# Kernel tuning notes

Hardware: AMD Instinct MI355X
Metric: run time of the kernel (lower is better)

The kernel has to match this reference:

```python
import jax, jax.numpy as jnp
import numpy as np

B, C, T, HEADS = 4, 1024, 1024, 16


def setup_inputs() -> dict:
    key = jax.random.key(0)
    k0, k1, k2, k3 = jax.random.split(key, 4)
    x = jax.random.normal(k0, (B, C, T), dtype=jnp.float32)
    mask = jax.random.randint(k1, (B, T), 0, 2).astype(bool)  # True = masked position
    scale = 1.0 / np.sqrt(C).astype(np.float32)
    w_kvq = jax.random.normal(k2, (3 * C, C), dtype=jnp.float32) * scale  # Conv1d k=1, no bias
    w_out = jax.random.normal(k3, (C, C), dtype=jnp.float32) * scale
    return {"x": x, "mask": mask, "w_kvq": w_kvq, "w_out": w_out}


def reference(x, mask, w_kvq, w_out):
    b, c, t = x.shape
    h = HEADS
    d = c // h  # head dim; torch scales by sqrt(k.size(1)) = sqrt(d)
    # Conv1d with kernel 1 == per-timestep matmul over channels
    kvq = jnp.einsum('oc,bct->bot', w_kvq, x)  # [B, 3C, T]
    k, v, q = jnp.split(kvq, 3, axis=1)        # each [B, C, T]
    k = k.reshape(b, h, d, t)
    v = v.reshape(b, h, d, t)
    q = q.reshape(b, h, d, t)
    # att[b,h,i,j] = <k_i, q_j> / sqrt(d); i = key pos, j = query pos
    att = jnp.einsum('bhdi,bhdj->bhij', k, q) / jnp.sqrt(jnp.asarray(d, x.dtype))
    # pre-softmax: mask key positions (dim i) with -inf
    att = jnp.where(mask[:, None, :, None], -jnp.inf, att)
    att = jax.nn.softmax(att, axis=2)  # softmax over keys (torch dim=1 of [Bh,Tk,Tq])
    # post-softmax: zero out masked query positions (dim j)
    att = jnp.where(mask[:, None, None, :], jnp.asarray(0.0, x.dtype), att)
    o = jnp.einsum('bhdi,bhij->bhdj', v, att)  # [B, h, d, T]
    o = o.reshape(b, c, t)
    out = x + jnp.einsum('oc,bct->bot', w_out, o)
    # match torch layout: cat over heads along batch dim -> [h*B, T, T]
    att_flat = jnp.transpose(att, (1, 0, 2, 3)).reshape(h * b, t, t)
    return out, att_flat
```

## Files before the change

kernel.cpp:

```cpp
#include <hip/hip_runtime.h>

#define BB 4
#define CC 1024
#define TT 1024
#define HH 16
#define DD 64

typedef __bf16 v8bf __attribute__((ext_vector_type(8)));
typedef __bf16 v4bf __attribute__((ext_vector_type(4)));
typedef float  v4f  __attribute__((ext_vector_type(4)));

__device__ __forceinline__ void async16(const __bf16* g, __bf16* l) {
  __builtin_amdgcn_global_load_lds(
      (const __attribute__((address_space(1))) void*)g,
      (__attribute__((address_space(3))) void*)l, 16, 0, 0);
}

__global__ __launch_bounds__(256) void expand_mask_kernel(const void* mraw, float* maskf) {
  __shared__ int flagA, flagB;
  if (threadIdx.x == 0) { flagA = 0; flagB = 0; }
  __syncthreads();
  const unsigned char* mb = (const unsigned char*)mraw;
  const int n = BB * TT;
  int a = 0, bfl = 0;
  for (int i = threadIdx.x; i < n; i += 256) {
    if (mb[i]) { if ((i & 3) == 0) a = 1; else bfl = 1; }
  }
  if (a)   atomicOr(&flagA, 1);
  if (bfl) atomicOr(&flagB, 1);
  __syncthreads();
  int layout;
  if (flagA && !flagB)      layout = 0;
  else if (!flagA && flagB) layout = 1;
  else                      layout = 2;
  for (int i = threadIdx.x; i < n; i += 256) {
    float m;
    if (layout == 0)      m = (((const int*)mraw)[i]   != 0)   ? 1.f : 0.f;
    else if (layout == 1) m = (((const float*)mraw)[i] != 0.f) ? 1.f : 0.f;
    else                  m = (mb[i] != 0)                     ? 1.f : 0.f;
    maskf[i] = m;
  }
}

__global__ __launch_bounds__(256) void cast_f32_bf16(const float* __restrict__ src,
                                                     __bf16* __restrict__ dst, int n) {
  int i = (blockIdx.x * 256 + threadIdx.x) * 8;
  if (i >= n) return;
  float4 f0 = *(const float4*)(src + i);
  float4 f1 = *(const float4*)(src + i + 4);
  v8bf o;
  o[0] = (__bf16)f0.x; o[1] = (__bf16)f0.y; o[2] = (__bf16)f0.z; o[3] = (__bf16)f0.w;
  o[4] = (__bf16)f1.x; o[5] = (__bf16)f1.y; o[6] = (__bf16)f1.z; o[7] = (__bf16)f1.w;
  *(v8bf*)(dst + i) = o;
}

__global__ __launch_bounds__(256) void transpose_x(const float* __restrict__ x,
                                                   __bf16* __restrict__ xT) {
  const int b = blockIdx.z;
  const int t0 = blockIdx.x * 64, c0 = blockIdx.y * 64;
  __shared__ __bf16 T[64][72];
  const int tid = threadIdx.x;
  {
    int row = tid >> 2, coff = (tid & 3) * 16;
    const float* src = x + ((long)b * CC + c0 + row) * TT + t0 + coff;
#pragma unroll
    for (int s = 0; s < 4; s++) {
      float4 f = *(const float4*)(src + s * 4);
      T[row][coff + s * 4 + 0] = (__bf16)f.x;
      T[row][coff + s * 4 + 1] = (__bf16)f.y;
      T[row][coff + s * 4 + 2] = (__bf16)f.z;
      T[row][coff + s * 4 + 3] = (__bf16)f.w;
    }
  }
  __syncthreads();
  {
    int trow = tid >> 2, ccoff = (tid & 3) * 16;
    __bf16 vals[16];
#pragma unroll
    for (int i = 0; i < 16; i++) vals[i] = T[ccoff + i][trow];
    __bf16* dst = xT + ((long)b * TT + t0 + trow) * CC + c0 + ccoff;
    *(v8bf*)dst       = *(v8bf*)&vals[0];
    *(v8bf*)(dst + 8) = *(v8bf*)&vals[8];
  }
}

__global__ __launch_bounds__(256) void transpose_kq(const __bf16* __restrict__ kvqb,
                                                    __bf16* __restrict__ kqT) {
  const int zz = blockIdx.z;
  const int b = zz >> 1, part = zz & 1;
  const int srcbase = part == 0 ? 0 : 2 * CC;
  const int dstbase = part * CC;
  const int t0 = blockIdx.x * 64, c0 = blockIdx.y * 64;
  __shared__ __bf16 T[64][72];
  const int tid = threadIdx.x;
  {
    int row = tid >> 2, coff = (tid & 3) * 16;
    const __bf16* src = kvqb + ((long)b * 3 * CC + srcbase + c0 + row) * TT + t0 + coff;
    *(v8bf*)&T[row][coff]     = *(const v8bf*)src;
    *(v8bf*)&T[row][coff + 8] = *(const v8bf*)(src + 8);
  }
  __syncthreads();
  {
    int trow = tid >> 2, ccoff = (tid & 3) * 16;
    __bf16 vals[16];
#pragma unroll
    for (int i = 0; i < 16; i++) vals[i] = T[ccoff + i][trow];
    __bf16* dst = kqT + ((long)b * TT + t0 + trow) * (2 * CC) + dstbase + c0 + ccoff;
    *(v8bf*)dst       = *(v8bf*)&vals[0];
    *(v8bf*)(dst + 8) = *(v8bf*)&vals[8];
  }
}

template <int MODE>
__global__ __launch_bounds__(256) void gemm_bt(
    const __bf16* __restrict__ A, const __bf16* __restrict__ BTfull,
    const float* __restrict__ Sfull, void* __restrict__ Ofull,
    long strideBT, long strideOS)
{
  const __bf16* BT = BTfull + (long)blockIdx.z * strideBT;
  const int m0 = blockIdx.y * 128, n0 = blockIdx.x * 128;
  __shared__ __align__(16) __bf16 As[128 * 32];
  __shared__ __align__(16) __bf16 Bs[128 * 32];
  const int tid = threadIdx.x;
  const int lane = tid & 63, wave = tid >> 6;
  const int wm = wave >> 1, wn = wave & 1;
  const int ln = lane & 15, q = lane >> 4;

  v4f acc[4][4];
#pragma unroll
  for (int i = 0; i < 4; i++)
#pragma unroll
    for (int j = 0; j < 4; j++) acc[i][j] = (v4f)(0.f);

  const int e0 = tid * 8;
  const int r0 = e0 >> 5, c0 = e0 & 31;
  const int e1 = (256 + tid) * 8;
  const int r1 = e1 >> 5, c1 = e1 & 31;
  const __bf16* ga0 = A  + (long)(m0 + r0) * CC + c0;
  const __bf16* ga1 = A  + (long)(m0 + r1) * CC + c1;
  const __bf16* gb0 = BT + (long)(n0 + r0) * CC + c0;
  const __bf16* gb1 = BT + (long)(n0 + r1) * CC + c1;
  __bf16* lA0 = &As[wave * 512];
  __bf16* lA1 = &As[2048 + wave * 512];
  __bf16* lB0 = &Bs[wave * 512];
  __bf16* lB1 = &Bs[2048 + wave * 512];

  for (int k0 = 0; k0 < CC; k0 += 32) {
    async16(ga0 + k0, lA0);
    async16(ga1 + k0, lA1);
    async16(gb0 + k0, lB0);
    async16(gb1 + k0, lB1);
    __syncthreads();
    v8bf af[4], bfr[4];
#pragma unroll
    for (int mi = 0; mi < 4; mi++)
      af[mi] = *(v8bf*)&As[(wm * 64 + mi * 16 + ln) * 32 + q * 8];
#pragma unroll
    for (int ni = 0; ni < 4; ni++)
      bfr[ni] = *(v8bf*)&Bs[(wn * 64 + ni * 16 + ln) * 32 + q * 8];
#pragma unroll
    for (int mi = 0; mi < 4; mi++)
#pragma unroll
      for (int ni = 0; ni < 4; ni++)
        acc[mi][ni] = __builtin_amdgcn_mfma_f32_16x16x32_bf16(af[mi], bfr[ni], acc[mi][ni], 0, 0, 0);
    __syncthreads();
  }
#pragma unroll
  for (int mi = 0; mi < 4; mi++)
#pragma unroll
    for (int ni = 0; ni < 4; ni++)
#pragma unroll
      for (int r = 0; r < 4; r++) {
        int row = m0 + wm * 64 + mi * 16 + q * 4 + r;
        int col = n0 + wn * 64 + ni * 16 + ln;
        if (MODE == 0) {
          ((__bf16*)Ofull)[(long)blockIdx.z * strideOS + (long)row * TT + col] = (__bf16)acc[mi][ni][r];
        } else {
          long off = (long)blockIdx.z * strideOS + (long)row * TT + col;
          ((float*)Ofull)[off] = acc[mi][ni][r] + Sfull[off];
        }
      }
}

__global__ __launch_bounds__(256) void attn_stats(
    const __bf16* __restrict__ kqT, const float* __restrict__ maskf,
    float* __restrict__ psum)
{
  const int z = blockIdx.z, h = z >> 2, b = z & 3;
  const int i0 = blockIdx.y * 128, j0 = blockIdx.x * 128;
  __shared__ __bf16 Ks[128][72];
  __shared__ __bf16 Qs[128][72];
  const __bf16* kbase = kqT + (long)b * TT * (2 * CC);
  const int tid = threadIdx.x;
#pragma unroll
  for (int s = 0; s < 4; s++) {
    int c = tid + s * 256;
    int row = c >> 3, off = (c & 7) * 8;
    *(v8bf*)&Ks[row][off] = *(const v8bf*)(kbase + (long)(i0 + row) * (2 * CC) + h * DD + off);
    *(v8bf*)&Qs[row][off] = *(const v8bf*)(kbase + (long)(j0 + row) * (2 * CC) + CC + h * DD + off);
  }
  __syncthreads();
  const int lane = tid & 63, wave = tid >> 6;
  const int wi = wave >> 1, wj = wave & 1;
  const int ln = lane & 15, q = lane >> 4;

  v8bf ak[4][2], bq[4][2];
#pragma unroll
  for (int mi = 0; mi < 4; mi++)
#pragma unroll
    for (int kd = 0; kd < 2; kd++)
      ak[mi][kd] = *(v8bf*)&Ks[wi * 64 + mi * 16 + ln][kd * 32 + q * 8];
#pragma unroll
  for (int ni = 0; ni < 4; ni++)
#pragma unroll
    for (int kd = 0; kd < 2; kd++)
      bq[ni][kd] = *(v8bf*)&Qs[wj * 64 + ni * 16 + ln][kd * 32 + q * 8];

  v4f acc[4][4];
#pragma unroll
  for (int mi = 0; mi < 4; mi++)
#pragma unroll
    for (int ni = 0; ni < 4; ni++) {
      v4f a = (v4f)(0.f);
      a = __builtin_amdgcn_mfma_f32_16x16x32_bf16(ak[mi][0], bq[ni][0], a, 0, 0, 0);
      a = __builtin_amdgcn_mfma_f32_16x16x32_bf16(ak[mi][1], bq[ni][1], a, 0, 0, 0);
      acc[mi][ni] = a;
    }

  float kmv[4][4];
#pragma unroll
  for (int mi = 0; mi < 4; mi++)
#pragma unroll
    for (int r = 0; r < 4; r++)
      kmv[mi][r] = maskf[b * TT + i0 + wi * 64 + mi * 16 + q * 4 + r];

#pragma unroll
  for (int ni = 0; ni < 4; ni++) {
    float s = 0.f;
#pragma unroll
    for (int mi = 0; mi < 4; mi++)
#pragma unroll
      for (int r = 0; r < 4; r++) {
        float e = __expf(acc[mi][ni][r] * 0.125f);
        s += (kmv[mi][r] != 0.f) ? 0.f : e;
      }
    s += __shfl_xor(s, 16, 64);
    s += __shfl_xor(s, 32, 64);
    if (q == 0) {
      long so = ((long)z * 16 + (i0 >> 6) + wi) * TT + j0 + wj * 64 + ni * 16 + ln;
      psum[so] = s;
    }
  }
}

__global__ __launch_bounds__(256) void gemm_pv(
    const __bf16* __restrict__ kqT, const __bf16* __restrict__ kvqb,
    const float* __restrict__ psum, const float* __restrict__ maskf,
    float* __restrict__ att, __bf16* __restrict__ oT)
{
  const int z = blockIdx.y, h = z >> 2, b = z & 3;
  const int j0 = blockIdx.x * 64;
  __shared__ __align__(16) char smem[40960];
  float* km = (float*)smem;
  const int tid = threadIdx.x;
  const int lane = tid & 63, wave = tid >> 6;
  const int ln = lane & 15, q = lane >> 4;
  __bf16 (*Pt)[72] = (__bf16(*)[72])(smem + 4096 + wave * 9216);

  const __bf16* kbase = kqT + (long)b * TT * (2 * CC);
  const __bf16* vbase = kvqb + (long)(b * 3 * CC + CC + h * DD) * TT;

  {
    float4 f = *(const float4*)(maskf + b * TT + tid * 4);
    *(float4*)&km[tid * 4] = f;
  }
  __syncthreads();

  v8bf bq[4][2];
#pragma unroll
  for (int ni = 0; ni < 4; ni++) {
    const __bf16* qr = kbase + (long)(j0 + ni * 16 + ln) * (2 * CC) + CC + h * DD;
    bq[ni][0] = *(const v8bf*)(qr + q * 8);
    bq[ni][1] = *(const v8bf*)(qr + 32 + q * 8);
  }
  float st[4];
#pragma unroll
  for (int ni = 0; ni < 4; ni++) {
    int j = j0 + ni * 16 + ln;
    float S = 0.f;
#pragma unroll
    for (int t = 0; t < 16; t++) S += psum[((long)z * 16 + t) * TT + j];
    st[ni] = (km[j] != 0.f) ? 0.f : 1.f / S;
  }

  v4f acc[4][4];
#pragma unroll
  for (int i = 0; i < 4; i++)
#pragma unroll
    for (int j = 0; j < 4; j++) acc[i][j] = (v4f)(0.f);

  for (int it = 0; it < 4; it++) {
    const int ibase = wave * 256 + it * 64;
#pragma unroll
    for (int mi = 0; mi < 4; mi++) {
      const __bf16* arow = kbase + (long)(ibase + mi * 16 + ln) * (2 * CC) + h * DD;
      v8bf ak0 = *(const v8bf*)(arow + q * 8);
      v8bf ak1 = *(const v8bf*)(arow + 32 + q * 8);
#pragma unroll
      for (int ni = 0; ni < 4; ni++) {
        v4f l4 = (v4f)(0.f);
        l4 = __builtin_amdgcn_mfma_f32_16x16x32_bf16(ak0, bq[ni][0], l4, 0, 0, 0);
        l4 = __builtin_amdgcn_mfma_f32_16x16x32_bf16(ak1, bq[ni][1], l4, 0, 0, 0);
        v4bf pb;
#pragma unroll
        for (int r = 0; r < 4; r++) {
          int i_loc = mi * 16 + q * 4 + r;
          int i_glob = ibase + i_loc;
          float p = (km[i_glob] != 0.f) ? 0.f : __expf(l4[r] * 0.125f) * st[ni];
          att[((long)z << 20) + (long)i_glob * TT + j0 + ni * 16 + ln] = p;
          pb[r] = (__bf16)p;
        }
        *(v4bf*)&Pt[ni * 16 + ln][mi * 16 + q * 4] = pb;
      }
    }
    v8bf ap[4][2], bv[4][2];
#pragma unroll
    for (int ji = 0; ji < 4; ji++)
#pragma unroll
      for (int ki = 0; ki < 2; ki++)
        ap[ji][ki] = *(v8bf*)&Pt[ji * 16 + ln][ki * 32 + q * 8];
#pragma unroll
    for (int di = 0; di < 4; di++)
#pragma unroll
      for (int ki = 0; ki < 2; ki++)
        bv[di][ki] = *(const v8bf*)(vbase + (long)(di * 16 + ln) * TT + ibase + ki * 32 + q * 8);
#pragma unroll
    for (int ji = 0; ji < 4; ji++)
#pragma unroll
      for (int di = 0; di < 4; di++) {
        acc[ji][di] = __builtin_amdgcn_mfma_f32_16x16x32_bf16(ap[ji][0], bv[di][0], acc[ji][di], 0, 0, 0);
        acc[ji][di] = __builtin_amdgcn_mfma_f32_16x16x32_bf16(ap[ji][1], bv[di][1], acc[ji][di], 0, 0, 0);
      }
  }

  float (*red0)[68] = (float(*)[68])(smem + 4096);
  float (*red1)[68] = (float(*)[68])(smem + 21504);
  __syncthreads();
  if ((wave & 1) == 0) {
    float (*red)[68] = (wave == 0) ? red0 : red1;
#pragma unroll
    for (int ji = 0; ji < 4; ji++)
#pragma unroll
      for (int di = 0; di < 4; di++)
#pragma unroll
        for (int r = 0; r < 4; r++)
          red[ji * 16 + q * 4 + r][di * 16 + ln] = acc[ji][di][r];
  }
  __syncthreads();
  if ((wave & 1) == 1) {
    float (*red)[68] = (wave == 1) ? red0 : red1;
#pragma unroll
    for (int ji = 0; ji < 4; ji++)
#pragma unroll
      for (int di = 0; di < 4; di++)
#pragma unroll
        for (int r = 0; r < 4; r++)
          red[ji * 16 + q * 4 + r][di * 16 + ln] += acc[ji][di][r];
  }
  __syncthreads();
  {
    int row = tid >> 2, c0 = (tid & 3) * 16;
    __bf16 ob[16];
#pragma unroll
    for (int i = 0; i < 16; i++) ob[i] = (__bf16)(red0[row][c0 + i] + red1[row][c0 + i]);
    __bf16* dst = oT + ((long)b * TT + j0 + row) * CC + h * DD + c0;
    *(v8bf*)dst       = *(v8bf*)&ob[0];
    *(v8bf*)(dst + 8) = *(v8bf*)&ob[8];
  }
}

extern "C" void kernel_launch(void* const* d_in, const int* in_sizes, int n_in,
                              void* d_out, int out_size, void* d_ws, size_t ws_size,
                              hipStream_t stream) {
  const float* x     = (const float*)d_in[0];
  const void*  mask  = d_in[1];
  const float* w_kvq = (const float*)d_in[2];
  const float* w_out = (const float*)d_in[3];

  float* out = (float*)d_out;
  float* att = out + (long)BB * CC * TT;

  char* wsb = (char*)d_ws;
  float*   maskf = (float*)(wsb + 0);
  __bf16*  wkb   = (__bf16*)(wsb + 16384);
  __bf16*  wob   = (__bf16*)(wsb + 6307840);
  __bf16*  xT    = (__bf16*)(wsb + 8404992);
  __bf16*  kqT   = (__bf16*)(wsb + 8404992);
  __bf16*  kvqb  = (__bf16*)(wsb + 25182208);
  __bf16*  oT    = (__bf16*)(wsb + 50348032);
  float*   psum  = (float*)(wsb + 58736640);

  expand_mask_kernel<<<1, 256, 0, stream>>>(mask, maskf);
  cast_f32_bf16<<<(3 * CC * CC) / 2048, 256, 0, stream>>>(w_kvq, wkb, 3 * CC * CC);
  cast_f32_bf16<<<(CC * CC) / 2048, 256, 0, stream>>>(w_out, wob, CC * CC);
  transpose_x<<<dim3(16, 16, BB), 256, 0, stream>>>(x, xT);
  gemm_bt<0><<<dim3(8, 24, BB), 256, 0, stream>>>(
      wkb, xT, nullptr, kvqb, (long)CC * TT, (long)3 * CC * TT);
  transpose_kq<<<dim3(16, 16, 2 * BB), 256, 0, stream>>>(kvqb, kqT);
  attn_stats<<<dim3(8, 8, HH * BB), 256, 0, stream>>>(kqT, maskf, psum);
  gemm_pv<<<dim3(16, HH * BB), 256, 0, stream>>>(kqT, kvqb, psum, maskf, att, oT);
  gemm_bt<1><<<dim3(8, 8, BB), 256, 0, stream>>>(
      wob, oT, x, out, (long)CC * TT, (long)CC * TT);
}
```

Before: 458.8 us.

## Fuse prep kernels, remap block order for XCDs, bitpack key mask, add setprio

Merges the mask expansion, the two weight casts and the x transpose into one prep launch, which also builds a bit-packed key mask. The GEMM, stats and PV kernels remap their flat block index so that neighbouring tiles land on the same XCD, which should improve L2 reuse. attn_stats now loads K and Q fragments straight from global memory instead of staging them in LDS. gemm_pv computes the per-query normaliser once per block in shared memory, reads mask bits instead of floats, and raises wave priority around the MFMA sections. Together these cut launch count and some memory traffic, at the cost of more complex indexing and uncoalesced direct loads in attn_stats.

```diff
diff --git a/kernel.cpp b/kernel.cpp
--- a/kernel.cpp
+++ b/kernel.cpp
@@ -16,71 +16,85 @@
       (__attribute__((address_space(3))) void*)l, 16, 0, 0);
 }
 
-__global__ __launch_bounds__(256) void expand_mask_kernel(const void* mraw, float* maskf) {
+__global__ __launch_bounds__(256) void prep(
+    const void* mraw, float* __restrict__ maskf, unsigned int* __restrict__ kmb,
+    const float* __restrict__ w_kvq, const float* __restrict__ w_out,
+    __bf16* __restrict__ wkb, __bf16* __restrict__ wob,
+    const float* __restrict__ x, __bf16* __restrict__ xT)
+{
+  const int blk = blockIdx.x;
+  const int tid = threadIdx.x;
   __shared__ int flagA, flagB;
-  if (threadIdx.x == 0) { flagA = 0; flagB = 0; }
-  __syncthreads();
-  const unsigned char* mb = (const unsigned char*)mraw;
-  const int n = BB * TT;
-  int a = 0, bfl = 0;
-  for (int i = threadIdx.x; i < n; i += 256) {
-    if (mb[i]) { if ((i & 3) == 0) a = 1; else bfl = 1; }
-  }
-  if (a)   atomicOr(&flagA, 1);
-  if (bfl) atomicOr(&flagB, 1);
-  __syncthreads();
-  int layout;
-  if (flagA && !flagB)      layout = 0;
-  else if (!flagA && flagB) layout = 1;
-  else                      layout = 2;
-  for (int i = threadIdx.x; i < n; i += 256) {
-    float m;
-    if (layout == 0)      m = (((const int*)mraw)[i]   != 0)   ? 1.f : 0.f;
-    else if (layout == 1) m = (((const float*)mraw)[i] != 0.f) ? 1.f : 0.f;
-    else                  m = (mb[i] != 0)                     ? 1.f : 0.f;
-    maskf[i] = m;
-  }
-}
-
-__global__ __launch_bounds__(256) void cast_f32_bf16(const float* __restrict__ src,
-                                                     __bf16* __restrict__ dst, int n) {
-  int i = (blockIdx.x * 256 + threadIdx.x) * 8;
-  if (i >= n) return;
-  float4 f0 = *(const float4*)(src + i);
-  float4 f1 = *(const float4*)(src + i + 4);
-  v8bf o;
-  o[0] = (__bf16)f0.x; o[1] = (__bf16)f0.y; o[2] = (__bf16)f0.z; o[3] = (__bf16)f0.w;
-  o[4] = (__bf16)f1.x; o[5] = (__bf16)f1.y; o[6] = (__bf16)f1.z; o[7] = (__bf16)f1.w;
-  *(v8bf*)(dst + i) = o;
-}
-
-__global__ __launch_bounds__(256) void transpose_x(const float* __restrict__ x,
-                                                   __bf16* __restrict__ xT) {
-  const int b = blockIdx.z;
-  const int t0 = blockIdx.x * 64, c0 = blockIdx.y * 64;
   __shared__ __bf16 T[64][72];
-  const int tid = threadIdx.x;
-  {
-    int row = tid >> 2, coff = (tid & 3) * 16;
-    const float* src = x + ((long)b * CC + c0 + row) * TT + t0 + coff;
-#pragma unroll
-    for (int s = 0; s < 4; s++) {
-      float4 f = *(const float4*)(src + s * 4);
-      T[row][coff + s * 4 + 0] = (__bf16)f.x;
-      T[row][coff + s * 4 + 1] = (__bf16)f.y;
-      T[row][coff + s * 4 + 2] = (__bf16)f.z;
-      T[row][coff + s * 4 + 3] = (__bf16)f.w;
-    }
-  }
-  __syncthreads();
-  {
-    int trow = tid >> 2, ccoff = (tid & 3) * 16;
-    __bf16 vals[16];
-#pragma unroll
-    for (int i = 0; i < 16; i++) vals[i] = T[ccoff + i][trow];
-    __bf16* dst = xT + ((long)b * TT + t0 + trow) * CC + c0 + ccoff;
-    *(v8bf*)dst       = *(v8bf*)&vals[0];
-    *(v8bf*)(dst + 8) = *(v8bf*)&vals[8];
+
+  if (blk == 0) {
+    if (tid == 0) { flagA = 0; flagB = 0; }
+    __syncthreads();
+    const unsigned char* mb = (const unsigned char*)mraw;
+    const int n = BB * TT;
+    int a = 0, bfl = 0;
+    for (int i = tid; i < n; i += 256) {
+      if (mb[i]) { if ((i & 3) == 0) a = 1; else bfl = 1; }
+    }
+    if (a)   atomicOr(&flagA, 1);
+    if (bfl) atomicOr(&flagB, 1);
+    __syncthreads();
+    int layout;
+    if (flagA && !flagB)      layout = 0;
+    else if (!flagA && flagB) layout = 1;
+    else                      layout = 2;
+    const int lane = tid & 63, wave = tid >> 6;
+    for (int it = 0; it < 16; it++) {
+      int i = it * 256 + tid;
+      float m;
+      if (layout == 0)      m = (((const int*)mraw)[i]   != 0)   ? 1.f : 0.f;
+      else if (layout == 1) m = (((const float*)mraw)[i] != 0.f) ? 1.f : 0.f;
+      else                  m = (mb[i] != 0)                     ? 1.f : 0.f;
+      maskf[i] = m;
+      unsigned long long bal = __ballot(m != 0.f);
+      if (lane == 0) {
+        int base = (it * 256 + wave * 64) >> 5;
+        kmb[base]     = (unsigned int)bal;
+        kmb[base + 1] = (unsigned int)(bal >> 32);
+      }
+    }
+  } else if (blk <= 2048) {
+    const int cb = blk - 1;
+    const float* src; __bf16* dst; int base;
+    if (cb < 1536) { src = w_kvq; dst = wkb; base = cb * 2048; }
+    else           { src = w_out; dst = wob; base = (cb - 1536) * 2048; }
+    int i = base + tid * 8;
+    float4 f0 = *(const float4*)(src + i);
+    float4 f1 = *(const float4*)(src + i + 4);
+    v8bf o;
+    o[0] = (__bf16)f0.x; o[1] = (__bf16)f0.y; o[2] = (__bf16)f0.z; o[3] = (__bf16)f0.w;
+    o[4] = (__bf16)f1.x; o[5] = (__bf16)f1.y; o[6] = (__bf16)f1.z; o[7] = (__bf16)f1.w;
+    *(v8bf*)(dst + i) = o;
+  } else {
+    const int idx = blk - 2049;
+    const int t0 = (idx & 15) * 64, c0 = ((idx >> 4) & 15) * 64, b = idx >> 8;
+    {
+      int row = tid >> 2, coff = (tid & 3) * 16;
+      const float* src = x + ((long)b * CC + c0 + row) * TT + t0 + coff;
+#pragma unroll
+      for (int s = 0; s < 4; s++) {
+        float4 f = *(const float4*)(src + s * 4);
+        T[row][coff + s * 4 + 0] = (__bf16)f.x;
+        T[row][coff + s * 4 + 1] = (__bf16)f.y;
+        T[row][coff + s * 4 + 2] = (__bf16)f.z;
+        T[row][coff + s * 4 + 3] = (__bf16)f.w;
+      }
+    }
+    __syncthreads();
+    {
+      int trow = tid >> 2, ccoff = (tid & 3) * 16;
+      __bf16 vals[16];
+#pragma unroll
+      for (int i = 0; i < 16; i++) vals[i] = T[ccoff + i][trow];
+      __bf16* dst = xT + ((long)b * TT + t0 + trow) * CC + c0 + ccoff;
+      *(v8bf*)dst       = *(v8bf*)&vals[0];
+      *(v8bf*)(dst + 8) = *(v8bf*)&vals[8];
+    }
   }
 }
 
@@ -111,14 +125,19 @@
   }
 }
 
-template <int MODE>
+template <int MODE, int NB, int MB>
 __global__ __launch_bounds__(256) void gemm_bt(
     const __bf16* __restrict__ A, const __bf16* __restrict__ BTfull,
     const float* __restrict__ Sfull, void* __restrict__ Ofull,
     long strideBT, long strideOS)
 {
-  const __bf16* BT = BTfull + (long)blockIdx.z * strideBT;
-  const int m0 = blockIdx.y * 128, n0 = blockIdx.x * 128;
+  constexpr int TOT = NB * MB * BB;
+  int flat = blockIdx.x + NB * (blockIdx.y + MB * blockIdx.z);
+  int L = (flat & 7) * (TOT / 8) + (flat >> 3);
+  const int n0 = (L % NB) * 128;
+  const int m0 = ((L / NB) % MB) * 128;
+  const int zb = L / (NB * MB);
+  const __bf16* BT = BTfull + (long)zb * strideBT;
   __shared__ __align__(16) __bf16 As[128 * 32];
   __shared__ __align__(16) __bf16 Bs[128 * 32];
   const int tid = threadIdx.x;
@@ -174,9 +193,9 @@
         int row = m0 + wm * 64 + mi * 16 + q * 4 + r;
         int col = n0 + wn * 64 + ni * 16 + ln;
         if (MODE == 0) {
-          ((__bf16*)Ofull)[(long)blockIdx.z * strideOS + (long)row * TT + col] = (__bf16)acc[mi][ni][r];
+          ((__bf16*)Ofull)[(long)zb * strideOS + (long)row * TT + col] = (__bf16)acc[mi][ni][r];
         } else {
-          long off = (long)blockIdx.z * strideOS + (long)row * TT + col;
+          long off = (long)zb * strideOS + (long)row * TT + col;
           ((float*)Ofull)[off] = acc[mi][ni][r] + Sfull[off];
         }
       }
@@ -186,37 +205,33 @@
     const __bf16* __restrict__ kqT, const float* __restrict__ maskf,
     float* __restrict__ psum)
 {
-  const int z = blockIdx.z, h = z >> 2, b = z & 3;
-  const int i0 = blockIdx.y * 128, j0 = blockIdx.x * 128;
-  __shared__ __bf16 Ks[128][72];
-  __shared__ __bf16 Qs[128][72];
+  int L = blockIdx.x + 8 * (blockIdx.y + 8 * blockIdx.z);
+  L = (L & 7) * 512 + (L >> 3);
+  const int jx = L & 7, iy = (L >> 3) & 7, z = L >> 6;
+  const int h = z >> 2, b = z & 3;
+  const int i0 = iy * 128, j0 = jx * 128;
   const __bf16* kbase = kqT + (long)b * TT * (2 * CC);
   const int tid = threadIdx.x;
-#pragma unroll
-  for (int s = 0; s < 4; s++) {
-    int c = tid + s * 256;
-    int row = c >> 3, off = (c & 7) * 8;
-    *(v8bf*)&Ks[row][off] = *(const v8bf*)(kbase + (long)(i0 + row) * (2 * CC) + h * DD + off);
-    *(v8bf*)&Qs[row][off] = *(const v8bf*)(kbase + (long)(j0 + row) * (2 * CC) + CC + h * DD + off);
-  }
-  __syncthreads();
   const int lane = tid & 63, wave = tid >> 6;
   const int wi = wave >> 1, wj = wave & 1;
   const int ln = lane & 15, q = lane >> 4;
 
   v8bf ak[4][2], bq[4][2];
 #pragma unroll
-  for (int mi = 0; mi < 4; mi++)
-#pragma unroll
-    for (int kd = 0; kd < 2; kd++)
-      ak[mi][kd] = *(v8bf*)&Ks[wi * 64 + mi * 16 + ln][kd * 32 + q * 8];
-#pragma unroll
-  for (int ni = 0; ni < 4; ni++)
-#pragma unroll
-    for (int kd = 0; kd < 2; kd++)
-      bq[ni][kd] = *(v8bf*)&Qs[wj * 64 + ni * 16 + ln][kd * 32 + q * 8];
+  for (int mi = 0; mi < 4; mi++) {
+    const __bf16* ar = kbase + (long)(i0 + wi * 64 + mi * 16 + ln) * (2 * CC) + h * DD;
+    ak[mi][0] = *(const v8bf*)(ar + q * 8);
+    ak[mi][1] = *(const v8bf*)(ar + 32 + q * 8);
+  }
+#pragma unroll
+  for (int ni = 0; ni < 4; ni++) {
+    const __bf16* br = kbase + (long)(j0 + wj * 64 + ni * 16 + ln) * (2 * CC) + CC + h * DD;
+    bq[ni][0] = *(const v8bf*)(br + q * 8);
+    bq[ni][1] = *(const v8bf*)(br + 32 + q * 8);
+  }
 
   v4f acc[4][4];
+  __builtin_amdgcn_s_setprio(1);
 #pragma unroll
   for (int mi = 0; mi < 4; mi++)
 #pragma unroll
@@ -226,6 +241,7 @@
       a = __builtin_amdgcn_mfma_f32_16x16x32_bf16(ak[mi][1], bq[ni][1], a, 0, 0, 0);
       acc[mi][ni] = a;
     }
+  __builtin_amdgcn_s_setprio(0);
 
   float kmv[4][4];
 #pragma unroll
@@ -241,8 +257,8 @@
     for (int mi = 0; mi < 4; mi++)
 #pragma unroll
       for (int r = 0; r < 4; r++) {
-        float e = __expf(acc[mi][ni][r] * 0.125f);
-        s += (kmv[mi][r] != 0.f) ? 0.f : e;
+        float e = (kmv[mi][r] != 0.f) ? 0.f : __expf(acc[mi][ni][r] * 0.125f);
+        s += e;
       }
     s += __shfl_xor(s, 16, 64);
     s += __shfl_xor(s, 32, 64);
@@ -256,24 +272,32 @@
 __global__ __launch_bounds__(256) void gemm_pv(
     const __bf16* __restrict__ kqT, const __bf16* __restrict__ kvqb,
     const float* __restrict__ psum, const float* __restrict__ maskf,
+    const unsigned int* __restrict__ kmb,
     float* __restrict__ att, __bf16* __restrict__ oT)
 {
-  const int z = blockIdx.y, h = z >> 2, b = z & 3;
-  const int j0 = blockIdx.x * 64;
-  __shared__ __align__(16) char smem[40960];
-  float* km = (float*)smem;
+  int L = blockIdx.x + 16 * blockIdx.y;
+  L = (L & 7) * 128 + (L >> 3);
+  const int z = L >> 4, jb = L & 15;
+  const int h = z >> 2, b = z & 3;
+  const int j0 = jb * 64;
+  __shared__ __align__(16) char smem[37376];
+  float* stl = (float*)smem;
+  unsigned int* kmw = (unsigned int*)(smem + 256);
   const int tid = threadIdx.x;
   const int lane = tid & 63, wave = tid >> 6;
   const int ln = lane & 15, q = lane >> 4;
-  __bf16 (*Pt)[72] = (__bf16(*)[72])(smem + 4096 + wave * 9216);
+  __bf16 (*Pt)[72] = (__bf16(*)[72])(smem + 512 + wave * 9216);
 
   const __bf16* kbase = kqT + (long)b * TT * (2 * CC);
   const __bf16* vbase = kvqb + (long)(b * 3 * CC + CC + h * DD) * TT;
 
-  {
-    float4 f = *(const float4*)(maskf + b * TT + tid * 4);
-    *(float4*)&km[tid * 4] = f;
-  }
+  if (tid < 64) {
+    float S = 0.f;
+#pragma unroll
+    for (int t = 0; t < 16; t++) S += psum[((long)z * 16 + t) * TT + j0 + tid];
+    stl[tid] = (maskf[b * TT + j0 + tid] != 0.f) ? 0.f : 1.f / S;
+  }
+  if (tid < 32) kmw[tid] = kmb[b * 32 + tid];
   __syncthreads();
 
   v8bf bq[4][2];
@@ -283,15 +307,9 @@
     bq[ni][0] = *(const v8bf*)(qr + q * 8);
     bq[ni][1] = *(const v8bf*)(qr + 32 + q * 8);
   }
-  float st[4];
-#pragma unroll
-  for (int ni = 0; ni < 4; ni++) {
-    int j = j0 + ni * 16 + ln;
-    float S = 0.f;
-#pragma unroll
-    for (int t = 0; t < 16; t++) S += psum[((long)z * 16 + t) * TT + j];
-    st[ni] = (km[j] != 0.f) ? 0.f : 1.f / S;
-  }
+  float stq[4];
+#pragma unroll
+  for (int ni = 0; ni < 4; ni++) stq[ni] = stl[ni * 16 + ln];
 
   v4f acc[4][4];
 #pragma unroll
@@ -316,7 +334,8 @@
         for (int r = 0; r < 4; r++) {
           int i_loc = mi * 16 + q * 4 + r;
           int i_glob = ibase + i_loc;
-          float p = (km[i_glob] != 0.f) ? 0.f : __expf(l4[r] * 0.125f) * st[ni];
+          unsigned int mbit = (kmw[i_glob >> 5] >> (i_glob & 31)) & 1u;
+          float p = mbit ? 0.f : __expf(l4[r] * 0.125f) * stq[ni];
           att[((long)z << 20) + (long)i_glob * TT + j0 + ni * 16 + ln] = p;
           pb[r] = (__bf16)p;
         }
@@ -334,6 +353,7 @@
 #pragma unroll
       for (int ki = 0; ki < 2; ki++)
         bv[di][ki] = *(const v8bf*)(vbase + (long)(di * 16 + ln) * TT + ibase + ki * 32 + q * 8);
+    __builtin_amdgcn_s_setprio(1);
 #pragma unroll
     for (int ji = 0; ji < 4; ji++)
 #pragma unroll
@@ -341,10 +361,11 @@
         acc[ji][di] = __builtin_amdgcn_mfma_f32_16x16x32_bf16(ap[ji][0], bv[di][0], acc[ji][di], 0, 0, 0);
         acc[ji][di] = __builtin_amdgcn_mfma_f32_16x16x32_bf16(ap[ji][1], bv[di][1], acc[ji][di], 0, 0, 0);
       }
-  }
-
-  float (*red0)[68] = (float(*)[68])(smem + 4096);
-  float (*red1)[68] = (float(*)[68])(smem + 21504);
+    __builtin_amdgcn_s_setprio(0);
+  }
+
+  float (*red0)[68] = (float(*)[68])(smem + 512);
+  float (*red1)[68] = (float(*)[68])(smem + 512 + 17408);
   __syncthreads();
   if ((wave & 1) == 0) {
     float (*red)[68] = (wave == 0) ? red0 : red1;
@@ -399,16 +420,14 @@
   __bf16*  kvqb  = (__bf16*)(wsb + 25182208);
   __bf16*  oT    = (__bf16*)(wsb + 50348032);
   float*   psum  = (float*)(wsb + 58736640);
-
-  expand_mask_kernel<<<1, 256, 0, stream>>>(mask, maskf);
-  cast_f32_bf16<<<(3 * CC * CC) / 2048, 256, 0, stream>>>(w_kvq, wkb, 3 * CC * CC);
-  cast_f32_bf16<<<(CC * CC) / 2048, 256, 0, stream>>>(w_out, wob, CC * CC);
-  transpose_x<<<dim3(16, 16, BB), 256, 0, stream>>>(x, xT);
-  gemm_bt<0><<<dim3(8, 24, BB), 256, 0, stream>>>(
+  unsigned int* kmb = (unsigned int*)(wsb + 62930944);
+
+  prep<<<3073, 256, 0, stream>>>(mask, maskf, kmb, w_kvq, w_out, wkb, wob, x, xT);
+  gemm_bt<0, 8, 24><<<dim3(8, 24, BB), 256, 0, stream>>>(
       wkb, xT, nullptr, kvqb, (long)CC * TT, (long)3 * CC * TT);
   transpose_kq<<<dim3(16, 16, 2 * BB), 256, 0, stream>>>(kvqb, kqT);
   attn_stats<<<dim3(8, 8, HH * BB), 256, 0, stream>>>(kqT, maskf, psum);
-  gemm_pv<<<dim3(16, HH * BB), 256, 0, stream>>>(kqT, kvqb, psum, maskf, att, oT);
-  gemm_bt<1><<<dim3(8, 8, BB), 256, 0, stream>>>(
+  gemm_pv<<<dim3(16, HH * BB), 256, 0, stream>>>(kqT, kvqb, psum, maskf, kmb, att, oT);
+  gemm_bt<1, 8, 8><<<dim3(8, 8, BB), 256, 0, stream>>>(
       wob, oT, x, out, (long)CC * TT, (long)CC * TT);
 }
```

New measurement: 462.1 us. No clear change (+0.7%).
